# Optimization experiments

Hardware: AMD Instinct MI355X
Metric: run time of the kernel (lower is better)

## Reference

```python
import jax, jax.numpy as jnp
import numpy as np

B, LQ, LK, E, H, F = 4, 1024, 1024, 1024, 16, 4096
DH = E // H
SCALE = 1.0 / float(np.sqrt(DH))


def _ln(x, g, b, eps=1e-5):
    m = jnp.mean(x, axis=-1, keepdims=True)
    v = jnp.mean((x - m) ** 2, axis=-1, keepdims=True)
    return (x - m) * jax.lax.rsqrt(v + eps) * g + b


def setup_inputs() -> dict:
    key = jax.random.key(0)
    ks = jax.random.split(key, 16)
    s = 0.02
    return {
        "tgt": jax.random.normal(ks[0], (B, LQ, E), jnp.float32),
        "memory": jax.random.normal(ks[1], (B, LK, E), jnp.float32),
        "ln1_g": jnp.ones((E,), jnp.float32),
        "ln1_b": jnp.zeros((E,), jnp.float32),
        "wq": jax.random.normal(ks[2], (E, E), jnp.float32) * s,
        "bq": jnp.zeros((E,), jnp.float32),
        "wk": jax.random.normal(ks[3], (E, E), jnp.float32) * s,
        "bk": jnp.zeros((E,), jnp.float32),
        "wv": jax.random.normal(ks[4], (E, E), jnp.float32) * s,
        "bv": jnp.zeros((E,), jnp.float32),
        "wo": jax.random.normal(ks[5], (E, E), jnp.float32) * s,
        "bo": jnp.zeros((E,), jnp.float32),
        "ln3_g": jnp.ones((E,), jnp.float32),
        "ln3_b": jnp.zeros((E,), jnp.float32),
        "w1": jax.random.normal(ks[6], (E, F), jnp.float32) * s,
        "b1": jnp.zeros((F,), jnp.float32),
        "w2": jax.random.normal(ks[7], (F, E), jnp.float32) * s,
        "b2": jnp.zeros((E,), jnp.float32),
    }


def reference(tgt, memory, ln1_g, ln1_b, wq, bq, wk, bk, wv, bv, wo, bo,
              ln3_g, ln3_b, w1, b1, w2, b2):
    # prenorm cross-attention (dropout=0 / eval mode)
    t2 = _ln(tgt, ln1_g, ln1_b)
    q = (t2 @ wq + bq).reshape(B, LQ, H, DH)
    k = (memory @ wk + bk).reshape(B, LK, H, DH)
    v = (memory @ wv + bv).reshape(B, LK, H, DH)
    scores = jnp.einsum('bqhd,bkhd->bhqk', q, k) * SCALE
    p = jax.nn.softmax(scores, axis=-1)          # [B,H,Lq,Lk]
    attn = jnp.mean(p, axis=1)                   # averaged over heads, like torch need_weights
    o = jnp.einsum('bhqk,bkhd->bqhd', p, v).reshape(B, LQ, E) @ wo + bo
    x = tgt + o
    # prenorm FFN
    t3 = _ln(x, ln3_g, ln3_b)
    ffn = jax.nn.relu(t3 @ w1 + b1) @ w2 + b2
    return x + ffn, attn
```

## Files before the change

kernel.cpp:

```cpp
#include <hip/hip_runtime.h>
#include <hip/hip_bf16.h>

using short8 = __attribute__((ext_vector_type(8))) short;
using f32x4  = __attribute__((ext_vector_type(4))) float;
using u16x4  = __attribute__((ext_vector_type(4))) unsigned short;

#define AS1 __attribute__((address_space(1)))
#define AS3 __attribute__((address_space(3)))

__device__ __forceinline__ unsigned short f2bf(float f) {
    __hip_bfloat16 h = __float2bfloat16(f);
    return __builtin_bit_cast(unsigned short, h);
}

__device__ __forceinline__ float exp2_hw(float x) {
    float r;
    asm("v_exp_f32 %0, %1" : "=v"(r) : "v"(x));
    return r;
}

__device__ __forceinline__ int vperm(int lk) {
    return (lk & ~31) | (((lk >> 2) & 3) * 8) | (((lk >> 4) & 1) * 4) | (lk & 3);
}

__global__ __launch_bounds__(256) void ln_to_bf16(
    const float* __restrict__ X, const float* __restrict__ gw,
    const float* __restrict__ bw, unsigned short* __restrict__ Y)
{
    const int row = blockIdx.x;
    const int tid = threadIdx.x;
    const float4 v = *(const float4*)(X + (size_t)row * 1024 + tid * 4);
    float s  = v.x + v.y + v.z + v.w;
    float s2 = v.x*v.x + v.y*v.y + v.z*v.z + v.w*v.w;
    #pragma unroll
    for (int off = 1; off < 64; off <<= 1) {
        s  += __shfl_xor(s,  off);
        s2 += __shfl_xor(s2, off);
    }
    __shared__ float rs[4], rq[4];
    if ((tid & 63) == 0) { rs[tid >> 6] = s; rq[tid >> 6] = s2; }
    __syncthreads();
    s  = rs[0] + rs[1] + rs[2] + rs[3];
    s2 = rq[0] + rq[1] + rq[2] + rq[3];
    const float mean = s * (1.f / 1024.f);
    const float var  = s2 * (1.f / 1024.f) - mean * mean;
    const float rstd = rsqrtf(var + 1e-5f);
    const float4 gv = *(const float4*)(gw + tid * 4);
    const float4 bv = *(const float4*)(bw + tid * 4);
    u16x4 o;
    o[0] = f2bf((v.x - mean) * rstd * gv.x + bv.x);
    o[1] = f2bf((v.y - mean) * rstd * gv.y + bv.y);
    o[2] = f2bf((v.z - mean) * rstd * gv.z + bv.z);
    o[3] = f2bf((v.w - mean) * rstd * gv.w + bv.w);
    *(u16x4*)(Y + (size_t)row * 1024 + tid * 4) = o;
}

__global__ __launch_bounds__(256) void prep_fused(
    const float* __restrict__ tgt, const float* __restrict__ ln1g,
    const float* __restrict__ ln1b, unsigned short* __restrict__ XA,
    const float* __restrict__ mem, unsigned short* __restrict__ M16,
    const float* __restrict__ wq, const float* __restrict__ wk,
    const float* __restrict__ wv, const float* __restrict__ wo,
    unsigned short* __restrict__ WQT, unsigned short* __restrict__ WKT,
    unsigned short* __restrict__ WVT, unsigned short* __restrict__ WOT,
    const float* __restrict__ w1, unsigned short* __restrict__ W1T,
    const float* __restrict__ w2, unsigned short* __restrict__ W2T)
{
    __shared__ float t[32][33];
    __shared__ float rs[4], rq[4];
    const int bid = blockIdx.x;
    const int tid = threadIdx.x;
    if (bid < 4096) {
        const int row = bid;
        const float4 v = *(const float4*)(tgt + (size_t)row * 1024 + tid * 4);
        float s  = v.x + v.y + v.z + v.w;
        float s2 = v.x*v.x + v.y*v.y + v.z*v.z + v.w*v.w;
        #pragma unroll
        for (int off = 1; off < 64; off <<= 1) {
            s  += __shfl_xor(s,  off);
            s2 += __shfl_xor(s2, off);
        }
        if ((tid & 63) == 0) { rs[tid >> 6] = s; rq[tid >> 6] = s2; }
        __syncthreads();
        s  = rs[0] + rs[1] + rs[2] + rs[3];
        s2 = rq[0] + rq[1] + rq[2] + rq[3];
        const float mean = s * (1.f / 1024.f);
        const float var  = s2 * (1.f / 1024.f) - mean * mean;
        const float rstd = rsqrtf(var + 1e-5f);
        const float4 gv = *(const float4*)(ln1g + tid * 4);
        const float4 bv = *(const float4*)(ln1b + tid * 4);
        u16x4 o;
        o[0] = f2bf((v.x - mean) * rstd * gv.x + bv.x);
        o[1] = f2bf((v.y - mean) * rstd * gv.y + bv.y);
        o[2] = f2bf((v.z - mean) * rstd * gv.z + bv.z);
        o[3] = f2bf((v.w - mean) * rstd * gv.w + bv.w);
        *(u16x4*)(XA + (size_t)row * 1024 + tid * 4) = o;
    } else if (bid < 8192) {
        const int i = (bid - 4096) * 256 + tid;
        float4 v = ((const float4*)mem)[i];
        u16x4 o = { f2bf(v.x), f2bf(v.y), f2bf(v.z), f2bf(v.w) };
        ((u16x4*)M16)[i] = o;
    } else {
        const float* W; unsigned short* Wt; int kb, nb, K;
        if (bid < 12288) {
            const int idx2 = bid - 8192;
            const int which = idx2 >> 10;
            W  = which == 0 ? wq : which == 1 ? wk : which == 2 ? wv : wo;
            Wt = which == 0 ? WQT : which == 1 ? WKT : which == 2 ? WVT : WOT;
            const int idx = idx2 & 1023;
            kb = idx & 31; nb = idx >> 5; K = 1024;
            const int c = tid & 31, r0 = tid >> 5;
            #pragma unroll
            for (int i = 0; i < 4; i++)
                t[r0 + i * 8][c] = W[(size_t)(kb * 32 + r0 + i * 8) * 1024 + nb * 32 + c];
            __syncthreads();
            #pragma unroll
            for (int i = 0; i < 4; i++)
                Wt[(size_t)(nb * 32 + r0 + i * 8) * K + kb * 32 + c] = f2bf(t[c][r0 + i * 8]);
        } else {
            int N;
            if (bid < 16384) { const int idx = bid - 12288; kb = idx % 32;  nb = idx / 32;  K = 1024; N = 4096; W = w1; Wt = W1T; }
            else             { const int idx = bid - 16384; kb = idx % 128; nb = idx / 128; K = 4096; N = 1024; W = w2; Wt = W2T; }
            const int c = tid & 31, r0 = tid >> 5;
            #pragma unroll
            for (int i = 0; i < 4; i++)
                t[r0 + i * 8][c] = W[(size_t)(kb * 32 + r0 + i * 8) * N + nb * 32 + c];
            __syncthreads();
            #pragma unroll
            for (int i = 0; i < 4; i++)
                Wt[(size_t)(nb * 32 + r0 + i * 8) * K + kb * 32 + c] = f2bf(t[c][r0 + i * 8]);
        }
    }
}

template<int EPI, int BN, int PF>
__device__ __forceinline__ void gemm_body(
    unsigned short* S,
    const unsigned short* __restrict__ A, const unsigned short* __restrict__ Bt,
    const float* __restrict__ bias, const float* __restrict__ bias2,
    void* __restrict__ outp, void* __restrict__ outp2,
    const float* __restrict__ resid, float oscale, int M, int N, int K,
    int vbid, int vgrid)
{
    constexpr int NF = BN / 32;
    constexpr int LDSH = (128 + BN) * 32;
    const int tid = threadIdx.x;
    const int lane = tid & 63, wave = tid >> 6;
    const int g = lane >> 4, q16 = lane & 15;
    const int wm = wave >> 1, wn = wave & 1;
    const int nb = N / BN;
    const int cpx = vgrid >> 3;
    const int swz = (vbid & 7) * cpx + (vbid >> 3);
    const int bm = swz / nb, bn = swz % nb;

    const unsigned short* aSrc = A  + (size_t)(bm * 128 + (tid >> 2)) * K + (tid & 3) * 8;
    const unsigned short* bSrc = Bt + (size_t)(bn * BN  + (tid >> 2)) * K + (tid & 3) * 8;
    const size_t rowStep = (size_t)64 * K;

    f32x4 acc[4][NF] = {};

    auto STAGE = [&](int slot, int kt) {
        unsigned short* aDst = &S[slot * LDSH] + wave * 512;
        unsigned short* bDst = &S[slot * LDSH + 4096] + wave * 512;
        __builtin_amdgcn_global_load_lds((const AS1 unsigned int*)(aSrc + kt),           (AS3 unsigned int*)aDst,          16, 0, 0);
        __builtin_amdgcn_global_load_lds((const AS1 unsigned int*)(aSrc + rowStep + kt), (AS3 unsigned int*)(aDst + 2048), 16, 0, 0);
        __builtin_amdgcn_global_load_lds((const AS1 unsigned int*)(bSrc + kt),           (AS3 unsigned int*)bDst,          16, 0, 0);
        if constexpr (BN == 128)
            __builtin_amdgcn_global_load_lds((const AS1 unsigned int*)(bSrc + rowStep + kt), (AS3 unsigned int*)(bDst + 2048), 16, 0, 0);
    };
    auto COMPUTE = [&](int slot) {
        const unsigned short* As = &S[slot * LDSH];
        const unsigned short* Bs = As + 4096;
        short8 af[4], bfr[NF];
        #pragma unroll
        for (int i = 0; i < 4; i++)  af[i]  = *(const short8*)(As + (wm * 64 + i * 16 + q16) * 32 + g * 8);
        #pragma unroll
        for (int i = 0; i < NF; i++) bfr[i] = *(const short8*)(Bs + (wn * (BN / 2) + i * 16 + q16) * 32 + g * 8);
        #pragma unroll
        for (int mf = 0; mf < 4; mf++)
            #pragma unroll
            for (int nf = 0; nf < NF; nf++)
                acc[mf][nf] = __builtin_amdgcn_mfma_f32_16x16x32_bf16(af[mf], bfr[nf], acc[mf][nf], 0, 0, 0);
    };

    #pragma unroll
    for (int i = 0; i < PF; i++) STAGE(i, i * 32);
    __syncthreads();
    int p = 0;
    #pragma unroll 1
    for (int kt = PF * 32; kt < K; kt += PF * 32) {
        #pragma unroll
        for (int i = 0; i < PF; i++) STAGE((p ^ 1) * PF + i, kt + i * 32);
        #pragma unroll
        for (int i = 0; i < PF; i++) COMPUTE(p * PF + i);
        __syncthreads();
        p ^= 1;
    }
    #pragma unroll
    for (int i = 0; i < PF; i++) COMPUTE(p * PF + i);

    const int row0 = bm * 128 + wm * 64;
    const int col0 = bn * BN + wn * (BN / 2);
    const bool isV = (EPI == 4) && (bn * BN >= 1024);
    #pragma unroll
    for (int nf = 0; nf < NF; nf++) {
        const int col = col0 + nf * 16 + q16;
        const float bv = (EPI == 4 && isV) ? bias2[col - 1024] : bias[col];
        #pragma unroll
        for (int mf = 0; mf < 4; mf++) {
            const int rbase = row0 + mf * 16 + g * 4;
            #pragma unroll
            for (int r = 0; r < 4; r++) {
                const int row = rbase + r;
                const float v = acc[mf][nf][r] + bv;
                if constexpr (EPI == 0) {
                    ((unsigned short*)outp)[(size_t)row * N + col] = f2bf(v * oscale);
                } else if constexpr (EPI == 1) {
                    const int bI = row >> 10, lk = row & 1023, hh = col >> 6, dd = col & 63;
                    ((unsigned short*)outp)[((size_t)(bI * 16 + hh) * 64 + dd) * 1024 + vperm(lk)] = f2bf(v);
                } else if constexpr (EPI == 2) {
                    ((unsigned short*)outp)[(size_t)row * N + col] = f2bf(v > 0.f ? v : 0.f);
                } else if constexpr (EPI == 3) {
                    ((float*)outp)[(size_t)row * N + col] = resid[(size_t)row * N + col] + v;
                } else {
                    if (!isV) {
                        ((unsigned short*)outp)[(size_t)row * 1024 + col] = f2bf(v);
                    } else {
                        const int cc = col - 1024;
                        const int bI = row >> 10, lk = row & 1023, hh = cc >> 6, dd = cc & 63;
                        ((unsigned short*)outp2)[((size_t)(bI * 16 + hh) * 64 + dd) * 1024 + vperm(lk)] = f2bf(v);
                    }
                }
            }
        }
    }
}

template<int EPI, int BN, int PF>
__global__ __launch_bounds__(256) void gemm_single(
    const unsigned short* __restrict__ A, const unsigned short* __restrict__ Bt,
    const float* __restrict__ bias, const float* __restrict__ bias2,
    void* __restrict__ outp, void* __restrict__ outp2,
    const float* __restrict__ resid, float oscale, int M, int N, int K)
{
    __shared__ unsigned short S[2 * PF * (128 + BN) * 32];
    gemm_body<EPI, BN, PF>(S, A, Bt, bias, bias2, outp, outp2, resid, oscale,
                           M, N, K, blockIdx.x, gridDim.x);
}

__global__ __launch_bounds__(256) void qkv_fused(
    const unsigned short* __restrict__ XA, const unsigned short* __restrict__ WQT,
    const float* __restrict__ bq,
    const unsigned short* __restrict__ M16, const unsigned short* __restrict__ WKT,
    const float* __restrict__ bk, const float* __restrict__ bv,
    unsigned short* __restrict__ Qb, unsigned short* __restrict__ Kb,
    unsigned short* __restrict__ Vt, float qscale)
{
    __shared__ unsigned short S[2 * 2 * 256 * 32];
    if (blockIdx.x < 512)
        gemm_body<0, 64, 2>(S, XA, WQT, bq, nullptr, Qb, nullptr, nullptr,
                            qscale, 4096, 1024, 1024, blockIdx.x, 512);
    else
        gemm_body<4, 128, 2>(S, M16, WKT, bk, bv, Kb, Vt, nullptr,
                             1.0f, 4096, 2048, 1024, blockIdx.x - 512, 512);
}

__global__ __launch_bounds__(256) void att_pv(
    const unsigned short* __restrict__ Q, const unsigned short* __restrict__ Kb,
    const unsigned short* __restrict__ Vt, unsigned short* __restrict__ O,
    float* __restrict__ LINV)
{
    __shared__ unsigned short Ks[2][2048];
    __shared__ unsigned short Vs[2][2048];
    const int tid = threadIdx.x, lane = tid & 63, wave = tid >> 6;
    const int g = lane >> 4, q16 = lane & 15;
    const int bh = blockIdx.x & 63;
    const int qt = blockIdx.x >> 6;
    const int b = bh >> 4, h = bh & 15;
    const int qbase = qt * 128 + wave * 32;

    const int rowK = wave * 8 + (lane >> 3);
    const int cK   = (lane & 7) ^ (rowK & 7);
    const int rowV = wave * 16 + (lane >> 2);
    const int cV   = (lane & 3) ^ (rowV & 3);
    const unsigned short* kSrc = Kb + ((size_t)(b * 1024 + rowK)) * 1024 + h * 64 + cK * 8;
    const unsigned short* vSrc = Vt + ((size_t)(bh * 64 + rowV)) * 1024 + cV * 8;

    short8 qf[2][2];
    #pragma unroll
    for (int nf = 0; nf < 2; nf++)
        #pragma unroll
        for (int ds = 0; ds < 2; ds++)
            qf[nf][ds] = *(const short8*)(Q + (size_t)(b * 1024 + qbase + nf * 16 + q16) * 1024 + h * 64 + ds * 32 + g * 8);

    f32x4 oacc[4][2] = {};
    float lsum[2] = {0.f, 0.f};

    auto STAGE = [&](int buf, int kc) {
        __builtin_amdgcn_global_load_lds((const AS1 unsigned int*)(kSrc + (size_t)kc * 1024),
                                         (AS3 unsigned int*)(&Ks[buf][0] + wave * 512), 16, 0, 0);
        __builtin_amdgcn_global_load_lds((const AS1 unsigned int*)(vSrc + kc),
                                         (AS3 unsigned int*)(&Vs[buf][0] + wave * 512), 16, 0, 0);
    };
    auto BODY = [&](int buf) {
        short8 kf[2][2], vf[4];
        #pragma unroll
        for (int kt = 0; kt < 2; kt++)
            #pragma unroll
            for (int ds = 0; ds < 2; ds++)
                kf[kt][ds] = *(const short8*)(&Ks[buf][0] + (kt * 16 + q16) * 64 + ((ds * 4 + g) ^ (q16 & 7)) * 8);
        #pragma unroll
        for (int mf = 0; mf < 4; mf++)
            vf[mf] = *(const short8*)(&Vs[buf][0] + (mf * 16 + q16) * 32 + (g ^ (q16 & 3)) * 8);
        f32x4 sacc[2][2] = {};
        #pragma unroll
        for (int kt = 0; kt < 2; kt++)
            #pragma unroll
            for (int nf = 0; nf < 2; nf++) {
                sacc[kt][nf] = __builtin_amdgcn_mfma_f32_16x16x32_bf16(kf[kt][0], qf[nf][0], sacc[kt][nf], 0, 0, 0);
                sacc[kt][nf] = __builtin_amdgcn_mfma_f32_16x16x32_bf16(kf[kt][1], qf[nf][1], sacc[kt][nf], 0, 0, 0);
            }
        float ps[2][2][4];
        #pragma unroll
        for (int kt = 0; kt < 2; kt++)
            #pragma unroll
            for (int nf = 0; nf < 2; nf++)
                #pragma unroll
                for (int r = 0; r < 4; r++)
                    ps[kt][nf][r] = exp2_hw(sacc[kt][nf][r]);
        #pragma unroll
        for (int nf = 0; nf < 2; nf++)
            lsum[nf] += ps[0][nf][0] + ps[0][nf][1] + ps[0][nf][2] + ps[0][nf][3]
                      + ps[1][nf][0] + ps[1][nf][1] + ps[1][nf][2] + ps[1][nf][3];
        short8 pbf[2];
        #pragma unroll
        for (int nf = 0; nf < 2; nf++) {
            pbf[nf][0] = (short)f2bf(ps[0][nf][0]);
            pbf[nf][1] = (short)f2bf(ps[0][nf][1]);
            pbf[nf][2] = (short)f2bf(ps[0][nf][2]);
            pbf[nf][3] = (short)f2bf(ps[0][nf][3]);
            pbf[nf][4] = (short)f2bf(ps[1][nf][0]);
            pbf[nf][5] = (short)f2bf(ps[1][nf][1]);
            pbf[nf][6] = (short)f2bf(ps[1][nf][2]);
            pbf[nf][7] = (short)f2bf(ps[1][nf][3]);
        }
        #pragma unroll
        for (int mf = 0; mf < 4; mf++)
            #pragma unroll
            for (int nf = 0; nf < 2; nf++)
                oacc[mf][nf] = __builtin_amdgcn_mfma_f32_16x16x32_bf16(vf[mf], pbf[nf], oacc[mf][nf], 0, 0, 0);
    };

    STAGE(0, 0);
    __syncthreads();
    int buf = 0;
    #pragma unroll 1
    for (int kc = 0; kc < 1024; kc += 32) {
        if (kc + 32 < 1024) STAGE(buf ^ 1, kc + 32);
        BODY(buf);
        __syncthreads();
        buf ^= 1;
    }
    #pragma unroll
    for (int nf = 0; nf < 2; nf++) {
        lsum[nf] += __shfl_xor(lsum[nf], 16);
        lsum[nf] += __shfl_xor(lsum[nf], 32);
    }

    #pragma unroll
    for (int nf = 0; nf < 2; nf++) {
        const float inv = 1.0f / lsum[nf];
        if (g == 0) LINV[(size_t)bh * 1024 + qbase + nf * 16 + q16] = inv;
        #pragma unroll
        for (int mf = 0; mf < 4; mf++) {
            u16x4 o;
            #pragma unroll
            for (int r = 0; r < 4; r++) o[r] = f2bf(oacc[mf][nf][r] * inv);
            *(u16x4*)(O + (size_t)(b * 1024 + qbase + nf * 16 + q16) * 1024 + h * 64 + mf * 16 + g * 4) = o;
        }
    }
}

__global__ __launch_bounds__(256) void att_mean(
    const unsigned short* __restrict__ Q, const unsigned short* __restrict__ Kb,
    const float* __restrict__ LINV, float* __restrict__ out1)
{
    __shared__ unsigned short Qs[2][2048];
    const int tid = threadIdx.x;
    const int lane = tid & 63, wave = tid >> 6;
    const int g = lane >> 4, q16 = lane & 15;
    const int kb = blockIdx.x & 7;
    const int qb = (blockIdx.x >> 3) & 31;
    const int b = blockIdx.x >> 8;
    const int qbase = qb * 32;
    const int kbase = kb * 128 + wave * 32;

    const int rowQ = wave * 8 + (lane >> 3);
    const int cQ   = (lane & 7) ^ (rowQ & 7);
    const unsigned short* qSrc = Q + (size_t)(b * 1024 + qbase + rowQ) * 1024 + cQ * 8;

    f32x4 facc[2][2] = {};

    auto STAGE = [&](int buf, int h) {
        __builtin_amdgcn_global_load_lds((const AS1 unsigned int*)(qSrc + h * 64),
                                         (AS3 unsigned int*)(&Qs[buf][0] + wave * 512), 16, 0, 0);
    };
    auto LOADK = [&](short8 (&kf)[2][2], f32x4 (&li)[2], int h) {
        #pragma unroll
        for (int nf = 0; nf < 2; nf++)
            #pragma unroll
            for (int ds = 0; ds < 2; ds++)
                kf[nf][ds] = *(const short8*)(Kb + (size_t)(b * 1024 + kbase + nf * 16 + q16) * 1024 + h * 64 + ds * 32 + g * 8);
        const float* lp = LINV + (size_t)(b * 16 + h) * 1024 + qbase;
        #pragma unroll
        for (int mf = 0; mf < 2; mf++)
            li[mf] = *(const f32x4*)(lp + mf * 16 + g * 4);
    };
    auto COMP = [&](int buf, short8 (&kf)[2][2], f32x4 (&li)[2]) {
        short8 qfr[2][2];
        #pragma unroll
        for (int mf = 0; mf < 2; mf++)
            #pragma unroll
            for (int ds = 0; ds < 2; ds++)
                qfr[mf][ds] = *(const short8*)(&Qs[buf][0] + (mf * 16 + q16) * 64 + ((ds * 4 + g) ^ (q16 & 7)) * 8);
        #pragma unroll
        for (int nf = 0; nf < 2; nf++) {
            f32x4 sacc[2] = {};
            #pragma unroll
            for (int mf = 0; mf < 2; mf++) {
                sacc[mf] = __builtin_amdgcn_mfma_f32_16x16x32_bf16(qfr[mf][0], kf[nf][0], sacc[mf], 0, 0, 0);
                sacc[mf] = __builtin_amdgcn_mfma_f32_16x16x32_bf16(qfr[mf][1], kf[nf][1], sacc[mf], 0, 0, 0);
            }
            #pragma unroll
            for (int mf = 0; mf < 2; mf++)
                #pragma unroll
                for (int r = 0; r < 4; r++)
                    facc[mf][nf][r] = fmaf(exp2_hw(sacc[mf][r]), li[mf][r], facc[mf][nf][r]);
        }
    };

    short8 kA[2][2], kB[2][2];
    f32x4 liA[2], liB[2];
    STAGE(0, 0); LOADK(kA, liA, 0);
    __syncthreads();
    #pragma unroll 1
    for (int h = 0; h < 16; h += 2) {
        STAGE(1, h + 1); LOADK(kB, liB, h + 1);
        COMP(0, kA, liA);
        __syncthreads();
        if (h + 2 < 16) { STAGE(0, h + 2); LOADK(kA, liA, h + 2); }
        COMP(1, kB, liB);
        __syncthreads();
    }

    #pragma unroll
    for (int mf = 0; mf < 2; mf++)
        #pragma unroll
        for (int nf = 0; nf < 2; nf++)
            #pragma unroll
            for (int r = 0; r < 4; r++)
                out1[(size_t)(b * 1024 + qbase + mf * 16 + g * 4 + r) * 1024 + kbase + nf * 16 + q16]
                    = facc[mf][nf][r] * 0.0625f;
}

extern "C" void kernel_launch(void* const* d_in, const int* in_sizes, int n_in,
                              void* d_out, int out_size, void* d_ws, size_t ws_size,
                              hipStream_t stream)
{
    (void)in_sizes; (void)n_in; (void)out_size; (void)ws_size;
    const float* tgt  = (const float*)d_in[0];
    const float* mem  = (const float*)d_in[1];
    const float* ln1g = (const float*)d_in[2];
    const float* ln1b = (const float*)d_in[3];
    const float* wq   = (const float*)d_in[4];
    const float* bq   = (const float*)d_in[5];
    const float* wk   = (const float*)d_in[6];
    const float* bk   = (const float*)d_in[7];
    const float* wv   = (const float*)d_in[8];
    const float* bv   = (const float*)d_in[9];
    const float* wo   = (const float*)d_in[10];
    const float* bo   = (const float*)d_in[11];
    const float* ln3g = (const float*)d_in[12];
    const float* ln3b = (const float*)d_in[13];
    const float* w1   = (const float*)d_in[14];
    const float* b1   = (const float*)d_in[15];
    const float* w2   = (const float*)d_in[16];
    const float* b2   = (const float*)d_in[17];

    char* ws = (char*)d_ws;
    unsigned short* XA  = (unsigned short*)(ws);
    unsigned short* M16 = (unsigned short*)(ws + ((size_t)8  << 20));
    unsigned short* WQT = (unsigned short*)(ws + ((size_t)16 << 20));
    unsigned short* WKT = (unsigned short*)(ws + ((size_t)18 << 20));
    unsigned short* WVT = (unsigned short*)(ws + ((size_t)20 << 20));
    unsigned short* WOT = (unsigned short*)(ws + ((size_t)22 << 20));
    unsigned short* W1T = (unsigned short*)(ws + ((size_t)24 << 20));
    unsigned short* W2T = (unsigned short*)(ws + ((size_t)32 << 20));
    unsigned short* Qb  = (unsigned short*)(ws + ((size_t)40 << 20));
    unsigned short* Kb  = (unsigned short*)(ws + ((size_t)48 << 20));
    unsigned short* Vt  = (unsigned short*)(ws + ((size_t)56 << 20));
    unsigned short* O16 = (unsigned short*)(ws + ((size_t)64 << 20));
    unsigned short* H16 = (unsigned short*)(ws + ((size_t)72 << 20));
    float*          LNV = (float*)(ws + ((size_t)104 << 20));
    float* xout = (float*)d_out;
    float* attn = xout + (size_t)4 * 1024 * 1024;

    const float QSCALE = 0.125f * 1.4426950408889634f;

    prep_fused<<<20480, 256, 0, stream>>>(tgt, ln1g, ln1b, XA, mem, M16,
                                          wq, wk, wv, wo, WQT, WKT, WVT, WOT,
                                          w1, W1T, w2, W2T);

    qkv_fused<<<1024, 256, 0, stream>>>(XA, WQT, bq, M16, WKT, bk, bv, Qb, Kb, Vt, QSCALE);

    att_pv<<<512, 256, 0, stream>>>(Qb, Kb, Vt, O16, LNV);
    att_mean<<<1024, 256, 0, stream>>>(Qb, Kb, LNV, attn);

    gemm_single<3, 64, 2><<<32 * 16, 256, 0, stream>>>(O16, WOT, bo, nullptr, xout, nullptr, tgt, 1.0f, 4096, 1024, 1024);
    ln_to_bf16<<<4096, 256, 0, stream>>>(xout, ln3g, ln3b, XA);
    gemm_single<2, 128, 2><<<32 * 32, 256, 0, stream>>>(XA, W1T, b1, nullptr, H16, nullptr, nullptr, 1.0f, 4096, 4096, 1024);
    gemm_single<3, 64, 2><<<32 * 16, 256, 0, stream>>>(H16, W2T, b2, nullptr, xout, nullptr, xout, 1.0f, 4096, 1024, 4096);
}
```

Baseline: 260.2 us.

## Use triple-buffered LDS ring with partial vmcnt waits for FFN down-projection GEMM

Adds a gemm_ring3 kernel that keeps three LDS stage-pairs in flight, so loads for tile t+2 are issued while tile t is computed. It waits with s_waitcnt vmcnt(N) plus a raw barrier instead of a full __syncthreads drain. The kernel replaces gemm_single for the K=4096 W2 GEMM, aiming to hide global-load latency over the long K loop. The epilogue is split into a shared helper. In exchange, LDS use per block rises by half, which may reduce occupancy, and the hand-counted vmcnt values must match the number of issued loads.

```diff
diff --git a/kernel.cpp b/kernel.cpp
--- a/kernel.cpp
+++ b/kernel.cpp
@@ -133,72 +133,14 @@
     }
 }
 
-template<int EPI, int BN, int PF>
-__device__ __forceinline__ void gemm_body(
-    unsigned short* S,
-    const unsigned short* __restrict__ A, const unsigned short* __restrict__ Bt,
+template<int EPI, int BN>
+__device__ __forceinline__ void gemm_epilogue(
+    f32x4 (&acc)[4][BN / 32], int bm, int bn, int wm, int wn, int g, int q16,
     const float* __restrict__ bias, const float* __restrict__ bias2,
     void* __restrict__ outp, void* __restrict__ outp2,
-    const float* __restrict__ resid, float oscale, int M, int N, int K,
-    int vbid, int vgrid)
+    const float* __restrict__ resid, float oscale, int N)
 {
     constexpr int NF = BN / 32;
-    constexpr int LDSH = (128 + BN) * 32;
-    const int tid = threadIdx.x;
-    const int lane = tid & 63, wave = tid >> 6;
-    const int g = lane >> 4, q16 = lane & 15;
-    const int wm = wave >> 1, wn = wave & 1;
-    const int nb = N / BN;
-    const int cpx = vgrid >> 3;
-    const int swz = (vbid & 7) * cpx + (vbid >> 3);
-    const int bm = swz / nb, bn = swz % nb;
-
-    const unsigned short* aSrc = A  + (size_t)(bm * 128 + (tid >> 2)) * K + (tid & 3) * 8;
-    const unsigned short* bSrc = Bt + (size_t)(bn * BN  + (tid >> 2)) * K + (tid & 3) * 8;
-    const size_t rowStep = (size_t)64 * K;
-
-    f32x4 acc[4][NF] = {};
-
-    auto STAGE = [&](int slot, int kt) {
-        unsigned short* aDst = &S[slot * LDSH] + wave * 512;
-        unsigned short* bDst = &S[slot * LDSH + 4096] + wave * 512;
-        __builtin_amdgcn_global_load_lds((const AS1 unsigned int*)(aSrc + kt),           (AS3 unsigned int*)aDst,          16, 0, 0);
-        __builtin_amdgcn_global_load_lds((const AS1 unsigned int*)(aSrc + rowStep + kt), (AS3 unsigned int*)(aDst + 2048), 16, 0, 0);
-        __builtin_amdgcn_global_load_lds((const AS1 unsigned int*)(bSrc + kt),           (AS3 unsigned int*)bDst,          16, 0, 0);
-        if constexpr (BN == 128)
-            __builtin_amdgcn_global_load_lds((const AS1 unsigned int*)(bSrc + rowStep + kt), (AS3 unsigned int*)(bDst + 2048), 16, 0, 0);
-    };
-    auto COMPUTE = [&](int slot) {
-        const unsigned short* As = &S[slot * LDSH];
-        const unsigned short* Bs = As + 4096;
-        short8 af[4], bfr[NF];
-        #pragma unroll
-        for (int i = 0; i < 4; i++)  af[i]  = *(const short8*)(As + (wm * 64 + i * 16 + q16) * 32 + g * 8);
-        #pragma unroll
-        for (int i = 0; i < NF; i++) bfr[i] = *(const short8*)(Bs + (wn * (BN / 2) + i * 16 + q16) * 32 + g * 8);
-        #pragma unroll
-        for (int mf = 0; mf < 4; mf++)
-            #pragma unroll
-            for (int nf = 0; nf < NF; nf++)
-                acc[mf][nf] = __builtin_amdgcn_mfma_f32_16x16x32_bf16(af[mf], bfr[nf], acc[mf][nf], 0, 0, 0);
-    };
-
-    #pragma unroll
-    for (int i = 0; i < PF; i++) STAGE(i, i * 32);
-    __syncthreads();
-    int p = 0;
-    #pragma unroll 1
-    for (int kt = PF * 32; kt < K; kt += PF * 32) {
-        #pragma unroll
-        for (int i = 0; i < PF; i++) STAGE((p ^ 1) * PF + i, kt + i * 32);
-        #pragma unroll
-        for (int i = 0; i < PF; i++) COMPUTE(p * PF + i);
-        __syncthreads();
-        p ^= 1;
-    }
-    #pragma unroll
-    for (int i = 0; i < PF; i++) COMPUTE(p * PF + i);
-
     const int row0 = bm * 128 + wm * 64;
     const int col0 = bn * BN + wn * (BN / 2);
     const bool isV = (EPI == 4) && (bn * BN >= 1024);
@@ -237,6 +179,76 @@
 }
 
 template<int EPI, int BN, int PF>
+__device__ __forceinline__ void gemm_body(
+    unsigned short* S,
+    const unsigned short* __restrict__ A, const unsigned short* __restrict__ Bt,
+    const float* __restrict__ bias, const float* __restrict__ bias2,
+    void* __restrict__ outp, void* __restrict__ outp2,
+    const float* __restrict__ resid, float oscale, int M, int N, int K,
+    int vbid, int vgrid)
+{
+    constexpr int NF = BN / 32;
+    constexpr int LDSH = (128 + BN) * 32;
+    const int tid = threadIdx.x;
+    const int lane = tid & 63, wave = tid >> 6;
+    const int g = lane >> 4, q16 = lane & 15;
+    const int wm = wave >> 1, wn = wave & 1;
+    const int nb = N / BN;
+    const int cpx = vgrid >> 3;
+    const int swz = (vbid & 7) * cpx + (vbid >> 3);
+    const int bm = swz / nb, bn = swz % nb;
+
+    const unsigned short* aSrc = A  + (size_t)(bm * 128 + (tid >> 2)) * K + (tid & 3) * 8;
+    const unsigned short* bSrc = Bt + (size_t)(bn * BN  + (tid >> 2)) * K + (tid & 3) * 8;
+    const size_t rowStep = (size_t)64 * K;
+
+    f32x4 acc[4][NF] = {};
+
+    auto STAGE = [&](int slot, int kt) {
+        unsigned short* aDst = &S[slot * LDSH] + wave * 512;
+        unsigned short* bDst = &S[slot * LDSH + 4096] + wave * 512;
+        __builtin_amdgcn_global_load_lds((const AS1 unsigned int*)(aSrc + kt),           (AS3 unsigned int*)aDst,          16, 0, 0);
+        __builtin_amdgcn_global_load_lds((const AS1 unsigned int*)(aSrc + rowStep + kt), (AS3 unsigned int*)(aDst + 2048), 16, 0, 0);
+        __builtin_amdgcn_global_load_lds((const AS1 unsigned int*)(bSrc + kt),           (AS3 unsigned int*)bDst,          16, 0, 0);
+        if constexpr (BN == 128)
+            __builtin_amdgcn_global_load_lds((const AS1 unsigned int*)(bSrc + rowStep + kt), (AS3 unsigned int*)(bDst + 2048), 16, 0, 0);
+    };
+    auto COMPUTE = [&](int slot) {
+        const unsigned short* As = &S[slot * LDSH];
+        const unsigned short* Bs = As + 4096;
+        short8 af[4], bfr[NF];
+        #pragma unroll
+        for (int i = 0; i < 4; i++)  af[i]  = *(const short8*)(As + (wm * 64 + i * 16 + q16) * 32 + g * 8);
+        #pragma unroll
+        for (int i = 0; i < NF; i++) bfr[i] = *(const short8*)(Bs + (wn * (BN / 2) + i * 16 + q16) * 32 + g * 8);
+        #pragma unroll
+        for (int mf = 0; mf < 4; mf++)
+            #pragma unroll
+            for (int nf = 0; nf < NF; nf++)
+                acc[mf][nf] = __builtin_amdgcn_mfma_f32_16x16x32_bf16(af[mf], bfr[nf], acc[mf][nf], 0, 0, 0);
+    };
+
+    #pragma unroll
+    for (int i = 0; i < PF; i++) STAGE(i, i * 32);
+    __syncthreads();
+    int p = 0;
+    #pragma unroll 1
+    for (int kt = PF * 32; kt < K; kt += PF * 32) {
+        #pragma unroll
+        for (int i = 0; i < PF; i++) STAGE((p ^ 1) * PF + i, kt + i * 32);
+        #pragma unroll
+        for (int i = 0; i < PF; i++) COMPUTE(p * PF + i);
+        __syncthreads();
+        p ^= 1;
+    }
+    #pragma unroll
+    for (int i = 0; i < PF; i++) COMPUTE(p * PF + i);
+
+    gemm_epilogue<EPI, BN>(acc, bm, bn, wm, wn, g, q16, bias, bias2,
+                           outp, outp2, resid, oscale, N);
+}
+
+template<int EPI, int BN, int PF>
 __global__ __launch_bounds__(256) void gemm_single(
     const unsigned short* __restrict__ A, const unsigned short* __restrict__ Bt,
     const float* __restrict__ bias, const float* __restrict__ bias2,
@@ -246,6 +258,81 @@
     __shared__ unsigned short S[2 * PF * (128 + BN) * 32];
     gemm_body<EPI, BN, PF>(S, A, Bt, bias, bias2, outp, outp2, resid, oscale,
                            M, N, K, blockIdx.x, gridDim.x);
+}
+
+template<int EPI, int BN, int PF>
+__global__ __launch_bounds__(256) void gemm_ring3(
+    const unsigned short* __restrict__ A, const unsigned short* __restrict__ Bt,
+    const float* __restrict__ bias, const float* __restrict__ bias2,
+    void* __restrict__ outp, void* __restrict__ outp2,
+    const float* __restrict__ resid, float oscale, int M, int N, int K)
+{
+    constexpr int NF = BN / 32;
+    constexpr int LDSH = (128 + BN) * 32;
+    constexpr int LPP = PF * (BN == 128 ? 4 : 3);
+    __shared__ unsigned short S[3 * PF * LDSH];
+    const int tid = threadIdx.x;
+    const int lane = tid & 63, wave = tid >> 6;
+    const int g = lane >> 4, q16 = lane & 15;
+    const int wm = wave >> 1, wn = wave & 1;
+    const int nb = N / BN;
+    const int cpx = gridDim.x >> 3;
+    const int swz = (blockIdx.x & 7) * cpx + (blockIdx.x >> 3);
+    const int bm = swz / nb, bn = swz % nb;
+
+    const unsigned short* aSrc = A  + (size_t)(bm * 128 + (tid >> 2)) * K + (tid & 3) * 8;
+    const unsigned short* bSrc = Bt + (size_t)(bn * BN  + (tid >> 2)) * K + (tid & 3) * 8;
+    const size_t rowStep = (size_t)64 * K;
+
+    f32x4 acc[4][NF] = {};
+
+    auto STAGEPAIR = [&](int pair, int t) {
+        #pragma unroll
+        for (int i = 0; i < PF; i++) {
+            const int kt = t * PF * 32 + i * 32;
+            unsigned short* aDst = &S[(pair * PF + i) * LDSH] + wave * 512;
+            unsigned short* bDst = &S[(pair * PF + i) * LDSH + 4096] + wave * 512;
+            __builtin_amdgcn_global_load_lds((const AS1 unsigned int*)(aSrc + kt),           (AS3 unsigned int*)aDst,          16, 0, 0);
+            __builtin_amdgcn_global_load_lds((const AS1 unsigned int*)(aSrc + rowStep + kt), (AS3 unsigned int*)(aDst + 2048), 16, 0, 0);
+            __builtin_amdgcn_global_load_lds((const AS1 unsigned int*)(bSrc + kt),           (AS3 unsigned int*)bDst,          16, 0, 0);
+            if constexpr (BN == 128)
+                __builtin_amdgcn_global_load_lds((const AS1 unsigned int*)(bSrc + rowStep + kt), (AS3 unsigned int*)(bDst + 2048), 16, 0, 0);
+        }
+    };
+    auto COMPUTEPAIR = [&](int pair) {
+        #pragma unroll
+        for (int s = 0; s < PF; s++) {
+            const unsigned short* As = &S[(pair * PF + s) * LDSH];
+            const unsigned short* Bs = As + 4096;
+            short8 af[4], bfr[NF];
+            #pragma unroll
+            for (int i = 0; i < 4; i++)  af[i]  = *(const short8*)(As + (wm * 64 + i * 16 + q16) * 32 + g * 8);
+            #pragma unroll
+            for (int i = 0; i < NF; i++) bfr[i] = *(const short8*)(Bs + (wn * (BN / 2) + i * 16 + q16) * 32 + g * 8);
+            #pragma unroll
+            for (int mf = 0; mf < 4; mf++)
+                #pragma unroll
+                for (int nf = 0; nf < NF; nf++)
+                    acc[mf][nf] = __builtin_amdgcn_mfma_f32_16x16x32_bf16(af[mf], bfr[nf], acc[mf][nf], 0, 0, 0);
+        }
+    };
+
+    const int NT = K / (PF * 32);
+    STAGEPAIR(0, 0);
+    STAGEPAIR(1, 1);
+    asm volatile("s_waitcnt vmcnt(%0)" :: "n"(LPP) : "memory");
+    __builtin_amdgcn_s_barrier();
+    #pragma unroll 1
+    for (int t = 0; t < NT; ++t) {
+        if (t + 2 < NT) STAGEPAIR((t + 2) % 3, t + 2);
+        COMPUTEPAIR(t % 3);
+        if (t + 1 < NT) asm volatile("s_waitcnt vmcnt(%0)" :: "n"(LPP) : "memory");
+        else            asm volatile("s_waitcnt vmcnt(0)" ::: "memory");
+        __builtin_amdgcn_s_barrier();
+    }
+
+    gemm_epilogue<EPI, BN>(acc, bm, bn, wm, wn, g, q16, bias, bias2,
+                           outp, outp2, resid, oscale, N);
 }
 
 __global__ __launch_bounds__(256) void qkv_fused(
@@ -519,5 +606,5 @@
     gemm_single<3, 64, 2><<<32 * 16, 256, 0, stream>>>(O16, WOT, bo, nullptr, xout, nullptr, tgt, 1.0f, 4096, 1024, 1024);
     ln_to_bf16<<<4096, 256, 0, stream>>>(xout, ln3g, ln3b, XA);
     gemm_single<2, 128, 2><<<32 * 32, 256, 0, stream>>>(XA, W1T, b1, nullptr, H16, nullptr, nullptr, 1.0f, 4096, 4096, 1024);
-    gemm_single<3, 64, 2><<<32 * 16, 256, 0, stream>>>(H16, W2T, b2, nullptr, xout, nullptr, xout, 1.0f, 4096, 1024, 4096);
-}
+    gemm_ring3<3, 64, 2><<<32 * 16, 256, 0, stream>>>(H16, W2T, b2, nullptr, xout, nullptr, xout, 1.0f, 4096, 1024, 4096);
+}
```

After: 261.3 us. About the same (+0.4%).
